# Kernel tuning notes

Measured on AMD Instinct MI355X. Metric: run time of the kernel, lower is better.

## Reference

```python
import jax, jax.numpy as jnp
import numpy as np

N, M, F, W = 600000, 300000, 128, 256  # points, masked points, grid feat_dim, net width


def _lin_init(k, fi, fo):
    k1, k2 = jax.random.split(k)
    s = 1.0 / np.sqrt(fi)
    return (jax.random.uniform(k1, (fi, fo), jnp.float32, -s, s),
            jax.random.uniform(k2, (fo,), jnp.float32, -s, s))


def setup_inputs() -> dict:
    key = jax.random.key(0)
    ks = jax.random.split(key, 24)
    # unique sorted indices emulate the boolean target_mask (static count M)
    idx = jnp.asarray(np.sort(np.random.RandomState(0).permutation(N)[:M]).astype(np.int32))
    inp = {
        "rays_pts_emb": jax.random.normal(ks[0], (N, 3), jnp.float32),
        "rotations_emb": jax.random.normal(ks[1], (N, 4), jnp.float32),
        "shs_emb": jax.random.normal(ks[2], (N, 16, 3), jnp.float32),
        "time_emb": jax.random.uniform(ks[3], (N, 1), jnp.float32),
        "h_emb": jax.random.uniform(ks[4], (N, 1), jnp.float32),
        "grid_sp": jax.random.normal(ks[5], (M, F), jnp.float32),
        "grid_st": jax.random.normal(ks[6], (M, F), jnp.float32),
        "idx": idx,
    }
    layers = [("sp", F, W), ("st", F, W), ("p1", W, W), ("p2", W, 9),
              ("r1", W, W), ("r2", W, 4), ("s1", W, W), ("s2", W, 48),
              ("w1", W, W), ("w2", W, 1), ("m1", W, W), ("m2", W, 1)]
    for i, (nm, fi, fo) in enumerate(layers):
        Wt, b = _lin_init(ks[7 + i], fi, fo)
        inp["W_" + nm] = Wt
        inp["b_" + nm] = b
    return inp


def _head(x, W1, b1, W2, b2):
    # nn.Sequential(ReLU, Linear, ReLU, Linear)
    h = jax.nn.relu(x)
    h = jax.nn.relu(h @ W1 + b1)
    return h @ W2 + b2


def reference(rays_pts_emb, rotations_emb, shs_emb, time_emb, h_emb, grid_sp, grid_st, idx,
              W_sp, b_sp, W_st, b_st, W_p1, b_p1, W_p2, b_p2, W_r1, b_r1, W_r2, b_r2,
              W_s1, b_s1, W_s2, b_s2, W_w1, b_w1, W_w2, b_w2, W_m1, b_m1, W_m2, b_m2):
    # encoders (Linear only, no activation)
    sp = grid_sp @ W_sp + b_sp            # [M, W]
    st = grid_st @ W_st + b_st            # [M, W]
    t = time_emb[0:1]                     # [1, 1]
    mint = 1.0 - t
    # position deformation: Bezier combination of 3 control offsets
    dx = _head(sp, W_p1, b_p1, W_p2, b_p2).reshape(-1, 3, 3)  # [M, 3, 3]
    delta = (3.0 * mint ** 2 * t * dx[:, 0]
             + 3.0 * mint * t ** 2 * dx[:, 1]
             + t ** 3 * dx[:, 2])                              # [M, 3]
    pts = rays_pts_emb.at[idx].add(delta)
    rotations = rotations_emb.at[idx].add(_head(st, W_r1, b_r1, W_r2, b_r2))
    shs = shs_emb.at[idx].add(_head(st, W_s1, b_s1, W_s2, b_s2).reshape(-1, 16, 3))
    # opacity gating
    w = _head(sp, W_w1, b_w1, W_w2, b_w2) ** 2                 # [M, 1]
    mu = jax.nn.sigmoid(_head(sp, W_m1, b_m1, W_m2, b_m2))     # [M, 1]
    opacity = h_emb.at[idx].set(h_emb[idx] * jnp.exp(-w * (t - mu) ** 2))
    return (pts, rotations, opacity, shs)
```

## Files before the change

### kernel.cpp

```cpp
#include <hip/hip_runtime.h>
#include <hip/hip_bf16.h>
#include <stdint.h>

#define M_ROWS 300000

typedef __attribute__((ext_vector_type(8)))  short bf16x8;
typedef __attribute__((ext_vector_type(16))) float f32x16;
typedef __attribute__((ext_vector_type(4)))  float f32x4;

union U4 { uint4 u; bf16x8 h; unsigned short us[8]; };

__device__ __forceinline__ unsigned short f2bf(float f) {
  union { float f; uint32_t u; } v; v.f = f;
  uint32_t r = v.u + 0x7fffu + ((v.u >> 16) & 1u);
  return (unsigned short)(r >> 16);
}
__device__ __forceinline__ uint32_t pk2(float lo, float hi) {
  return (uint32_t)f2bf(lo) | ((uint32_t)f2bf(hi) << 16);
}
__device__ __forceinline__ f32x4 ntload4(const float* p) {
  return __builtin_nontemporal_load((const f32x4*)p);
}
__device__ __forceinline__ void ntstore4(float* p, f32x4 v) {
  __builtin_nontemporal_store(v, (f32x4*)p);
}

#define T_SP 0
#define T_ST 64
#define T_P1 128
#define T_P2 256
#define T_R1 272
#define T_R2 400
#define T_S1 416
#define T_S2 544
#define T_W1 576
#define T_W2 704
#define T_M1 720
#define T_M2 848
#define T_TOT 864

__global__ void prep_w(const float* Wsp, const float* Wst, const float* Wp1, const float* Wp2,
                       const float* Wr1, const float* Wr2, const float* Ws1, const float* Ws2,
                       const float* Ww1, const float* Ww2, const float* Wm1, const float* Wm2,
                       uint4* ws) {
  int b = blockIdx.x, l = threadIdx.x;
  const int starts[12] = {T_SP,T_ST,T_P1,T_P2,T_R1,T_R2,T_S1,T_S2,T_W1,T_W2,T_M1,T_M2};
  const int Ks[12]     = {128,128,256,256,256,256,256,256,256,256,256,256};
  const int Cos[12]    = {256,256,256,9,256,4,256,48,256,1,256,1};
  const float* Wp[12]  = {Wsp,Wst,Wp1,Wp2,Wr1,Wr2,Ws1,Ws2,Ww1,Ww2,Wm1,Wm2};
  int m = 0;
  #pragma unroll
  for (int i = 1; i < 12; ++i) if (b >= starts[i]) m = i;
  int local = b - starts[m];
  int KT = Ks[m] >> 4;
  int n0 = local / KT, k0 = local - n0 * KT;
  int col = n0 * 32 + (l & 31);
  int kbase = k0 * 16 + (l >> 5) * 8;
  const float* W = Wp[m];
  int Co = Cos[m];
  U4 pk;
  #pragma unroll
  for (int j = 0; j < 8; ++j) {
    float v = (col < Co) ? W[(size_t)(kbase + j) * Co + col] : 0.0f;
    pk.us[j] = f2bf(v);
  }
  ws[(size_t)b * 64 + l] = pk.u;
}

__global__ void copy_emb(const float* pts, const float* rot, const float* h,
                         const float* shs, float* out) {
  long long stride = (long long)gridDim.x * blockDim.x;
  for (long long i = (long long)blockIdx.x * blockDim.x + threadIdx.x; i < 8400000LL; i += stride) {
    if (i < 450000) {
      ntstore4(out + i * 4, ntload4(pts + i * 4));
    } else if (i < 1050000) {
      f32x4 v = ntload4(rot + (i - 450000) * 4);
      *(f32x4*)(out + i * 4) = v;
    } else if (i < 1200000) {
      ntstore4(out + i * 4, ntload4(h + (i - 1050000) * 4));
    } else {
      f32x4 v = ntload4(shs + (i - 1200000) * 4);
      *(f32x4*)(out + i * 4) = v;
    }
  }
}

#define LSTR 512
__device__ __forceinline__ int lds_addr(int row, int cb) {
  return row * LSTR + (cb ^ ((row & 15) << 4));
}

__device__ __forceinline__ void loadX(const float* grid, int row0, int t, char* buf) {
  #pragma unroll
  for (int i = 0; i < 4; ++i) {
    int fi = i * 512 + t;
    int row = fi >> 5;
    int c4 = fi & 31;
    int gr = row0 + row; gr = gr < M_ROWS ? gr : (M_ROWS - 1);
    f32x4 v = ntload4(grid + (size_t)gr * 128 + c4 * 4);
    ushort4 p;
    p.x = f2bf(v.x); p.y = f2bf(v.y); p.z = f2bf(v.z); p.w = f2bf(v.w);
    *(ushort4*)(buf + lds_addr(row, c4 * 8)) = p;
  }
}

__device__ __forceinline__ void pre8(U4 (&d)[8], const uint4* base, int lane) {
  #pragma unroll
  for (int i = 0; i < 8; ++i) d[i].u = base[(size_t)i * 64 + lane];
}
__device__ __forceinline__ void pre4(U4 (&d)[8], const uint4* base, int lane) {
  #pragma unroll
  for (int i = 0; i < 4; ++i) d[i].u = base[(size_t)i * 64 + lane];
}
__device__ __forceinline__ void pre_s2(U4 (&d)[8], const uint4* wt, int kq, int lane) {
  #pragma unroll
  for (int kk = 0; kk < 4; ++kk)
    #pragma unroll
    for (int n = 0; n < 2; ++n)
      d[kk * 2 + n].u = wt[(size_t)((n * 16 + kq * 4 + kk) * 64) + lane];
}

__device__ __forceinline__ void mm_big8T(U4 (&b)[8], const char* inb, int k0, int arow, int khalf,
                                         f32x16& acc0, f32x16& acc1) {
  #pragma unroll
  for (int k = 0; k < 8; ++k) {
    bf16x8 x0 = *(const bf16x8*)(inb + lds_addr(arow, (k0 + k) * 32 + khalf));
    bf16x8 x1 = *(const bf16x8*)(inb + lds_addr(32 + arow, (k0 + k) * 32 + khalf));
    acc0 = __builtin_amdgcn_mfma_f32_32x32x16_bf16(b[k].h, x0, acc0, 0, 0, 0);
    acc1 = __builtin_amdgcn_mfma_f32_32x32x16_bf16(b[k].h, x1, acc1, 0, 0, 0);
  }
}

__device__ __forceinline__ void store_actT(char* outb, const float* bias, int wave, int lane,
                                           const f32x16& acc0, const f32x16& acc1) {
  const int xr = lane & 31;
  const int cb0 = wave * 32 + 4 * (lane >> 5);
  #pragma unroll
  for (int run = 0; run < 4; ++run) {
    const int c0 = cb0 + 8 * run;
    const float4 bv = *(const float4*)(bias + c0);
    uint2 w0, w1;
    w0.x = pk2(fmaxf(acc0[run * 4 + 0] + bv.x, 0.0f), fmaxf(acc0[run * 4 + 1] + bv.y, 0.0f));
    w0.y = pk2(fmaxf(acc0[run * 4 + 2] + bv.z, 0.0f), fmaxf(acc0[run * 4 + 3] + bv.w, 0.0f));
    w1.x = pk2(fmaxf(acc1[run * 4 + 0] + bv.x, 0.0f), fmaxf(acc1[run * 4 + 1] + bv.y, 0.0f));
    w1.y = pk2(fmaxf(acc1[run * 4 + 2] + bv.z, 0.0f), fmaxf(acc1[run * 4 + 3] + bv.w, 0.0f));
    *(uint2*)(outb + lds_addr(xr, c0 * 2)) = w0;
    *(uint2*)(outb + lds_addr(32 + xr, c0 * 2)) = w1;
  }
}

__device__ __forceinline__ void mm_head1(U4 (&b)[8], const char* inb, int rg, int kq, int khalf,
                                         int lane, f32x16& acc) {
  const int arow = rg * 32 + (lane & 31);
  #pragma unroll
  for (int kk = 0; kk < 4; ++kk) {
    bf16x8 a = *(const bf16x8*)(inb + lds_addr(arow, (kq * 4 + kk) * 32 + khalf));
    acc = __builtin_amdgcn_mfma_f32_32x32x16_bf16(a, b[kk].h, acc, 0, 0, 0);
  }
}

template<int COLS>
__device__ __forceinline__ void head_atomic(float* outsm, int rg, int lane, const f32x16& acc) {
  int col = lane & 31;
  if (col < COLS) {
    #pragma unroll
    for (int q = 0; q < 16; ++q) {
      int row = rg * 32 + (q & 3) + 8 * (q >> 2) + 4 * (lane >> 5);
      atomicAdd(&outsm[row * COLS + col], acc[q]);
    }
  }
}

__device__ __forceinline__ void rot_atomic_global(const f32x16& acc, int rg, int kq, int lane,
                                                  const int* sidx, int row0, const float* b_r2,
                                                  float* out) {
  int col = lane & 31;
  if (col < 4) {
    float bb = (kq == 0) ? b_r2[col] : 0.0f;
    #pragma unroll
    for (int q = 0; q < 16; ++q) {
      int row = rg * 32 + (q & 3) + 8 * (q >> 2) + 4 * (lane >> 5);
      if (row0 + row < M_ROWS) {
        atomicAdd(out + 1800000 + (size_t)sidx[row] * 4 + col, acc[q] + bb);
      }
    }
  }
}

__device__ __forceinline__ void shs_atomic_global(const f32x16& a0, const f32x16& a1,
                                                  int rg, int kq, int lane,
                                                  const int* sidx, int row0, const float* b_s2,
                                                  float* out) {
  int c = lane & 31;
  float bb0 = (kq == 0) ? b_s2[c] : 0.0f;
  float bb1 = (kq == 0 && c < 16) ? b_s2[32 + c] : 0.0f;
  #pragma unroll
  for (int q = 0; q < 16; ++q) {
    int row = rg * 32 + (q & 3) + 8 * (q >> 2) + 4 * (lane >> 5);
    if (row0 + row < M_ROWS) {
      size_t base = 4800000 + (size_t)sidx[row] * 48;
      atomicAdd(out + base + c, a0[q] + bb0);
      if (c < 16) atomicAdd(out + base + 32 + c, a1[q] + bb1);
    }
  }
}

__global__ void __launch_bounds__(512, 4) deform_main(
    const float* grid_sp, const float* grid_st, const int* idx,
    const float* rays, const float* rotq, const float* shs_in,
    const float* time_emb, const float* h_emb,
    const uint4* ws,
    const float* b_sp, const float* b_st, const float* b_p1, const float* b_p2,
    const float* b_r1, const float* b_r2, const float* b_s1, const float* b_s2,
    const float* b_w1, const float* b_w2, const float* b_m1, const float* b_m2,
    float* out) {
  __shared__ char bufA[32768];
  __shared__ char bufB[32768];
  __shared__ float smf[704];
  __shared__ int sidx[64];
  float* dxb = smf;
  float* wb  = smf + 576;
  float* mub = smf + 640;

  const int t = threadIdx.x;
  const int lane = t & 63;
  const int wave = t >> 6;
  const int rg = wave & 1;
  const int kq = wave >> 1;
  const int arow = lane & 31;
  const int khalf = (lane >> 5) * 16;
  const int row0 = blockIdx.x * 64;
  const float tt = time_emb[0];

  U4 b0[8], b1[8];
  pre8(b0, ws + (size_t)(T_SP + wave * 8) * 64, lane);

  if (t < 64) { int gr = row0 + t; sidx[t] = idx[gr < M_ROWS ? gr : (M_ROWS - 1)]; }
  if (t < 512) smf[t] = 0.0f;
  if (t < 192) smf[512 + t] = 0.0f;
  loadX(grid_sp, row0, t, bufA);
  __syncthreads();

  {
    f32x16 a0 = (f32x16)0.0f, a1 = (f32x16)0.0f;
    pre8(b1, ws + (size_t)(T_P1 + wave * 16) * 64, lane);
    __builtin_amdgcn_s_setprio(1);
    mm_big8T(b0, bufA, 0, arow, khalf, a0, a1);
    __builtin_amdgcn_s_setprio(0);
    store_actT(bufB, b_sp, wave, lane, a0, a1);
  }
  __syncthreads();

  {
    f32x16 a0 = (f32x16)0.0f, a1 = (f32x16)0.0f;
    pre8(b0, ws + (size_t)(T_P1 + wave * 16 + 8) * 64, lane);
    __builtin_amdgcn_s_setprio(1);
    mm_big8T(b1, bufB, 0, arow, khalf, a0, a1);
    __builtin_amdgcn_s_setprio(0);
    pre4(b1, ws + (size_t)(T_P2 + kq * 4) * 64, lane);
    __builtin_amdgcn_s_setprio(1);
    mm_big8T(b0, bufB, 8, arow, khalf, a0, a1);
    __builtin_amdgcn_s_setprio(0);
    store_actT(bufA, b_p1, wave, lane, a0, a1);
  }
  __syncthreads();

  {
    f32x16 hacc = (f32x16)0.0f;
    pre8(b0, ws + (size_t)(T_W1 + wave * 16) * 64, lane);
    __builtin_amdgcn_s_setprio(1);
    mm_head1(b1, bufA, rg, kq, khalf, lane, hacc);
    __builtin_amdgcn_s_setprio(0);
    head_atomic<9>(dxb, rg, lane, hacc);
  }
  __syncthreads();

  {
    f32x16 a0 = (f32x16)0.0f, a1 = (f32x16)0.0f;
    pre8(b1, ws + (size_t)(T_W1 + wave * 16 + 8) * 64, lane);
    __builtin_amdgcn_s_setprio(1);
    mm_big8T(b0, bufB, 0, arow, khalf, a0, a1);
    __builtin_amdgcn_s_setprio(0);
    pre4(b0, ws + (size_t)(T_W2 + kq * 4) * 64, lane);
    __builtin_amdgcn_s_setprio(1);
    mm_big8T(b1, bufB, 8, arow, khalf, a0, a1);
    __builtin_amdgcn_s_setprio(0);
    store_actT(bufA, b_w1, wave, lane, a0, a1);
  }
  __syncthreads();

  {
    f32x16 hacc = (f32x16)0.0f;
    pre8(b1, ws + (size_t)(T_M1 + wave * 16) * 64, lane);
    __builtin_amdgcn_s_setprio(1);
    mm_head1(b0, bufA, rg, kq, khalf, lane, hacc);
    __builtin_amdgcn_s_setprio(0);
    head_atomic<1>(wb, rg, lane, hacc);
  }
  __syncthreads();

  {
    f32x16 a0 = (f32x16)0.0f, a1 = (f32x16)0.0f;
    pre8(b0, ws + (size_t)(T_M1 + wave * 16 + 8) * 64, lane);
    __builtin_amdgcn_s_setprio(1);
    mm_big8T(b1, bufB, 0, arow, khalf, a0, a1);
    __builtin_amdgcn_s_setprio(0);
    pre4(b1, ws + (size_t)(T_M2 + kq * 4) * 64, lane);
    __builtin_amdgcn_s_setprio(1);
    mm_big8T(b0, bufB, 8, arow, khalf, a0, a1);
    __builtin_amdgcn_s_setprio(0);
    store_actT(bufA, b_m1, wave, lane, a0, a1);
  }
  __syncthreads();

  float pr = 0.0f, hv = 0.0f;
  {
    if (t < 256) {
      int row = t >> 2, sub = t & 3;
      int g = sidx[row];
      if (sub < 3) pr = rays[(size_t)g * 3 + sub]; else hv = h_emb[g];
    }
    loadX(grid_st, row0, t, bufB);
    f32x16 hacc = (f32x16)0.0f;
    __builtin_amdgcn_s_setprio(1);
    mm_head1(b1, bufA, rg, kq, khalf, lane, hacc);
    __builtin_amdgcn_s_setprio(0);
    pre8(b0, ws + (size_t)(T_ST + wave * 8) * 64, lane);
    head_atomic<1>(mub, rg, lane, hacc);
  }
  __syncthreads();

  {
    f32x16 a0 = (f32x16)0.0f, a1 = (f32x16)0.0f;
    pre8(b1, ws + (size_t)(T_R1 + wave * 16) * 64, lane);
    __builtin_amdgcn_s_setprio(1);
    mm_big8T(b0, bufB, 0, arow, khalf, a0, a1);
    __builtin_amdgcn_s_setprio(0);
    store_actT(bufA, b_st, wave, lane, a0, a1);
    if (t < 256) {
      int row = t >> 2, sub = t & 3;
      int gr = row0 + row;
      if (gr < M_ROWS) {
        int g = sidx[row];
        if (sub < 3) {
          float mt = 1.0f - tt;
          float c0 = 3.0f * mt * mt * tt, c1 = 3.0f * mt * tt * tt, c2 = tt * tt * tt;
          float d0 = dxb[row * 9 + sub]     + b_p2[sub];
          float d1 = dxb[row * 9 + 3 + sub] + b_p2[3 + sub];
          float d2 = dxb[row * 9 + 6 + sub] + b_p2[6 + sub];
          __builtin_nontemporal_store(pr + (c0 * d0 + c1 * d1 + c2 * d2),
                                      out + (size_t)g * 3 + sub);
        } else {
          float wr = wb[row] + b_w2[0];
          float mr = mub[row] + b_m2[0];
          float mu = 1.0f / (1.0f + expf(-mr));
          float dtm = tt - mu;
          __builtin_nontemporal_store(hv * expf(-(wr * wr) * dtm * dtm),
                                      out + 4200000 + (size_t)g);
        }
      }
    }
  }
  __syncthreads();

  {
    f32x16 a0 = (f32x16)0.0f, a1 = (f32x16)0.0f;
    pre8(b0, ws + (size_t)(T_R1 + wave * 16 + 8) * 64, lane);
    __builtin_amdgcn_s_setprio(1);
    mm_big8T(b1, bufA, 0, arow, khalf, a0, a1);
    __builtin_amdgcn_s_setprio(0);
    pre4(b1, ws + (size_t)(T_R2 + kq * 4) * 64, lane);
    __builtin_amdgcn_s_setprio(1);
    mm_big8T(b0, bufA, 8, arow, khalf, a0, a1);
    __builtin_amdgcn_s_setprio(0);
    store_actT(bufB, b_r1, wave, lane, a0, a1);
  }
  __syncthreads();

  {
    f32x16 hacc = (f32x16)0.0f;
    pre8(b0, ws + (size_t)(T_S1 + wave * 16) * 64, lane);
    __builtin_amdgcn_s_setprio(1);
    mm_head1(b1, bufB, rg, kq, khalf, lane, hacc);
    __builtin_amdgcn_s_setprio(0);
    rot_atomic_global(hacc, rg, kq, lane, sidx, row0, b_r2, out);
  }
  __syncthreads();

  {
    f32x16 a0 = (f32x16)0.0f, a1 = (f32x16)0.0f;
    pre8(b1, ws + (size_t)(T_S1 + wave * 16 + 8) * 64, lane);
    __builtin_amdgcn_s_setprio(1);
    mm_big8T(b0, bufA, 0, arow, khalf, a0, a1);
    __builtin_amdgcn_s_setprio(0);
    pre_s2(b0, ws + (size_t)T_S2 * 64, kq, lane);
    __builtin_amdgcn_s_setprio(1);
    mm_big8T(b1, bufA, 8, arow, khalf, a0, a1);
    __builtin_amdgcn_s_setprio(0);
    store_actT(bufB, b_s1, wave, lane, a0, a1);
  }
  __syncthreads();

  {
    f32x16 h0 = (f32x16)0.0f, h1 = (f32x16)0.0f;
    const int ar = rg * 32 + (lane & 31);
    __builtin_amdgcn_s_setprio(1);
    #pragma unroll
    for (int kk = 0; kk < 4; ++kk) {
      bf16x8 a = *(const bf16x8*)(bufB + lds_addr(ar, (kq * 4 + kk) * 32 + khalf));
      h0 = __builtin_amdgcn_mfma_f32_32x32x16_bf16(a, b0[kk * 2 + 0].h, h0, 0, 0, 0);
      h1 = __builtin_amdgcn_mfma_f32_32x32x16_bf16(a, b0[kk * 2 + 1].h, h1, 0, 0, 0);
    }
    __builtin_amdgcn_s_setprio(0);
    shs_atomic_global(h0, h1, rg, kq, lane, sidx, row0, b_s2, out);
  }
}

extern "C" void kernel_launch(void* const* d_in, const int* in_sizes, int n_in,
                              void* d_out, int out_size, void* d_ws, size_t ws_size,
                              hipStream_t stream) {
  const float* rays     = (const float*)d_in[0];
  const float* rotq     = (const float*)d_in[1];
  const float* shs      = (const float*)d_in[2];
  const float* time_emb = (const float*)d_in[3];
  const float* h_emb    = (const float*)d_in[4];
  const float* grid_sp  = (const float*)d_in[5];
  const float* grid_st  = (const float*)d_in[6];
  const int*   idx      = (const int*)d_in[7];
  uint4* ws = (uint4*)d_ws;

  prep_w<<<T_TOT, 64, 0, stream>>>(
      (const float*)d_in[8],  (const float*)d_in[10], (const float*)d_in[12], (const float*)d_in[14],
      (const float*)d_in[16], (const float*)d_in[18], (const float*)d_in[20], (const float*)d_in[22],
      (const float*)d_in[24], (const float*)d_in[26], (const float*)d_in[28], (const float*)d_in[30],
      ws);

  copy_emb<<<2048, 256, 0, stream>>>(rays, rotq, h_emb, shs, (float*)d_out);

  deform_main<<<(M_ROWS + 63) / 64, 512, 0, stream>>>(
      grid_sp, grid_st, idx, rays, rotq, shs, time_emb, h_emb, ws,
      (const float*)d_in[9],  (const float*)d_in[11], (const float*)d_in[13], (const float*)d_in[15],
      (const float*)d_in[17], (const float*)d_in[19], (const float*)d_in[21], (const float*)d_in[23],
      (const float*)d_in[25], (const float*)d_in[27], (const float*)d_in[29], (const float*)d_in[31],
      (float*)d_out);
}
```

Baseline: 708.1 us.

## Fuse passthrough embedding copies into main kernel using a mask bitmap

```diff
diff --git a/kernel.cpp b/kernel.cpp
--- a/kernel.cpp
+++ b/kernel.cpp
@@ -3,6 +3,7 @@
 #include <stdint.h>
 
 #define M_ROWS 300000
+#define NB_DEF 4688
 
 typedef __attribute__((ext_vector_type(8)))  short bf16x8;
 typedef __attribute__((ext_vector_type(16))) float f32x16;
@@ -23,6 +24,9 @@
 }
 __device__ __forceinline__ void ntstore4(float* p, f32x4 v) {
   __builtin_nontemporal_store(v, (f32x4*)p);
+}
+__device__ __forceinline__ bool bit_set(const uint32_t* bm, int r) {
+  return (bm[r >> 5] >> (r & 31)) & 1u;
 }
 
 #define T_SP 0
@@ -67,22 +71,10 @@
   ws[(size_t)b * 64 + l] = pk.u;
 }
 
-__global__ void copy_emb(const float* pts, const float* rot, const float* h,
-                         const float* shs, float* out) {
-  long long stride = (long long)gridDim.x * blockDim.x;
-  for (long long i = (long long)blockIdx.x * blockDim.x + threadIdx.x; i < 8400000LL; i += stride) {
-    if (i < 450000) {
-      ntstore4(out + i * 4, ntload4(pts + i * 4));
-    } else if (i < 1050000) {
-      f32x4 v = ntload4(rot + (i - 450000) * 4);
-      *(f32x4*)(out + i * 4) = v;
-    } else if (i < 1200000) {
-      ntstore4(out + i * 4, ntload4(h + (i - 1050000) * 4));
-    } else {
-      f32x4 v = ntload4(shs + (i - 1200000) * 4);
-      *(f32x4*)(out + i * 4) = v;
-    }
-  }
+__global__ void bm_zero(uint32_t* bm) { bm[blockIdx.x * 256 + threadIdx.x] = 0u; }
+__global__ void bm_set(const int* idx, uint32_t* bm) {
+  int i = blockIdx.x * 256 + threadIdx.x;
+  if (i < M_ROWS) { int g = idx[i]; atomicOr(&bm[g >> 5], 1u << (g & 31)); }
 }
 
 #define LSTR 512
@@ -209,7 +201,7 @@
     const float* grid_sp, const float* grid_st, const int* idx,
     const float* rays, const float* rotq, const float* shs_in,
     const float* time_emb, const float* h_emb,
-    const uint4* ws,
+    const uint4* ws, const uint32_t* bm,
     const float* b_sp, const float* b_st, const float* b_p1, const float* b_p2,
     const float* b_r1, const float* b_r2, const float* b_s1, const float* b_s2,
     const float* b_w1, const float* b_w2, const float* b_m1, const float* b_m2,
@@ -229,7 +221,8 @@
   const int kq = wave >> 1;
   const int arow = lane & 31;
   const int khalf = (lane >> 5) * 16;
-  const int row0 = blockIdx.x * 64;
+  const int bid = blockIdx.x;
+  const int row0 = bid * 64;
   const float tt = time_emb[0];
 
   U4 b0[8], b1[8];
@@ -244,6 +237,22 @@
   {
     f32x16 a0 = (f32x16)0.0f, a1 = (f32x16)0.0f;
     pre8(b1, ws + (size_t)(T_P1 + wave * 16) * 64, lane);
+    if (t < 64 && row0 + t < M_ROWS) {
+      int g = sidx[t];
+      *(float4*)(out + 1800000 + (size_t)g * 4) = *(const float4*)(rotq + (size_t)g * 4);
+    }
+    #pragma unroll
+    for (int i = 0; i < 2; ++i) {
+      int e = i * 512 + t;
+      if (e < 768) {
+        int r = e / 12, c = e - r * 12;
+        if (row0 + r < M_ROWS) {
+          int g = sidx[r];
+          *(float4*)(out + 4800000 + (size_t)g * 48 + c * 4) =
+              *(const float4*)(shs_in + (size_t)g * 48 + c * 4);
+        }
+      }
+    }
     __builtin_amdgcn_s_setprio(1);
     mm_big8T(b0, bufA, 0, arow, khalf, a0, a1);
     __builtin_amdgcn_s_setprio(0);
@@ -254,6 +263,20 @@
   {
     f32x16 a0 = (f32x16)0.0f, a1 = (f32x16)0.0f;
     pre8(b0, ws + (size_t)(T_P1 + wave * 16 + 8) * 64, lane);
+    {
+      long long c0 = (long long)bid * 1536;
+      #pragma unroll
+      for (int i = 0; i < 2; ++i) {
+        int j = i * 512 + t;
+        if (j < 768) {
+          long long c = c0 + j;
+          if (c < 7200000) {
+            int r = (int)(c / 12);
+            if (!bit_set(bm, r)) ntstore4(out + 4800000 + c * 4, ntload4(shs_in + c * 4));
+          }
+        }
+      }
+    }
     __builtin_amdgcn_s_setprio(1);
     mm_big8T(b1, bufB, 0, arow, khalf, a0, a1);
     __builtin_amdgcn_s_setprio(0);
@@ -278,6 +301,20 @@
   {
     f32x16 a0 = (f32x16)0.0f, a1 = (f32x16)0.0f;
     pre8(b1, ws + (size_t)(T_W1 + wave * 16 + 8) * 64, lane);
+    {
+      long long c0 = (long long)bid * 1536 + 768;
+      #pragma unroll
+      for (int i = 0; i < 2; ++i) {
+        int j = i * 512 + t;
+        if (j < 768) {
+          long long c = c0 + j;
+          if (c < 7200000) {
+            int r = (int)(c / 12);
+            if (!bit_set(bm, r)) ntstore4(out + 4800000 + c * 4, ntload4(shs_in + c * 4));
+          }
+        }
+      }
+    }
     __builtin_amdgcn_s_setprio(1);
     mm_big8T(b0, bufB, 0, arow, khalf, a0, a1);
     __builtin_amdgcn_s_setprio(0);
@@ -302,6 +339,21 @@
   {
     f32x16 a0 = (f32x16)0.0f, a1 = (f32x16)0.0f;
     pre8(b0, ws + (size_t)(T_M1 + wave * 16 + 8) * 64, lane);
+    if (t < 384) {
+      long long e = (long long)bid * 384 + t;
+      if (e < 1800000) {
+        int r = (int)(e / 3);
+        if (!bit_set(bm, r))
+          __builtin_nontemporal_store(__builtin_nontemporal_load(rays + e), out + e);
+      }
+    }
+    if (t < 128) {
+      long long c = (long long)bid * 128 + t;
+      if (c < 600000) {
+        int r = (int)c;
+        if (!bit_set(bm, r)) ntstore4(out + 1800000 + c * 4, ntload4(rotq + c * 4));
+      }
+    }
     __builtin_amdgcn_s_setprio(1);
     mm_big8T(b1, bufB, 0, arow, khalf, a0, a1);
     __builtin_amdgcn_s_setprio(0);
@@ -319,6 +371,15 @@
       int row = t >> 2, sub = t & 3;
       int g = sidx[row];
       if (sub < 3) pr = rays[(size_t)g * 3 + sub]; else hv = h_emb[g];
+    }
+    if (t >= 256 && t < 384) {
+      long long e = (long long)bid * 128 + (t - 256);
+      if (e < 600000) {
+        int r = (int)e;
+        if (!bit_set(bm, r))
+          __builtin_nontemporal_store(__builtin_nontemporal_load(h_emb + e),
+                                      out + 4200000 + e);
+      }
     }
     loadX(grid_st, row0, t, bufB);
     f32x16 hacc = (f32x16)0.0f;
@@ -428,6 +489,7 @@
   const float* grid_st  = (const float*)d_in[6];
   const int*   idx      = (const int*)d_in[7];
   uint4* ws = (uint4*)d_ws;
+  uint32_t* bm = (uint32_t*)((char*)d_ws + (size_t)T_TOT * 1024);
 
   prep_w<<<T_TOT, 64, 0, stream>>>(
       (const float*)d_in[8],  (const float*)d_in[10], (const float*)d_in[12], (const float*)d_in[14],
@@ -435,10 +497,11 @@
       (const float*)d_in[24], (const float*)d_in[26], (const float*)d_in[28], (const float*)d_in[30],
       ws);
 
-  copy_emb<<<2048, 256, 0, stream>>>(rays, rotq, h_emb, shs, (float*)d_out);
-
-  deform_main<<<(M_ROWS + 63) / 64, 512, 0, stream>>>(
-      grid_sp, grid_st, idx, rays, rotq, shs, time_emb, h_emb, ws,
+  bm_zero<<<75, 256, 0, stream>>>(bm);
+  bm_set<<<(M_ROWS + 255) / 256, 256, 0, stream>>>(idx, bm);
+
+  deform_main<<<NB_DEF, 512, 0, stream>>>(
+      grid_sp, grid_st, idx, rays, rotq, shs, time_emb, h_emb, ws, bm,
       (const float*)d_in[9],  (const float*)d_in[11], (const float*)d_in[13], (const float*)d_in[15],
       (const float*)d_in[17], (const float*)d_in[19], (const float*)d_in[21], (const float*)d_in[23],
       (const float*)d_in[25], (const float*)d_in[27], (const float*)d_in[29], (const float*)d_in[31],
```

New measurement: 944.4 us. 1.33x slower.

## Halve block row tile to 32 rows and repartition head work across waves

Applied to the files above, without the earlier changes.

```diff
diff --git a/kernel.cpp b/kernel.cpp
--- a/kernel.cpp
+++ b/kernel.cpp
@@ -92,12 +92,11 @@
 
 __device__ __forceinline__ void loadX(const float* grid, int row0, int t, char* buf) {
   #pragma unroll
-  for (int i = 0; i < 4; ++i) {
+  for (int i = 0; i < 2; ++i) {
     int fi = i * 512 + t;
     int row = fi >> 5;
     int c4 = fi & 31;
-    int gr = row0 + row; gr = gr < M_ROWS ? gr : (M_ROWS - 1);
-    f32x4 v = ntload4(grid + (size_t)gr * 128 + c4 * 4);
+    f32x4 v = ntload4(grid + (size_t)(row0 + row) * 128 + c4 * 4);
     ushort4 p;
     p.x = f2bf(v.x); p.y = f2bf(v.y); p.z = f2bf(v.z); p.w = f2bf(v.w);
     *(ushort4*)(buf + lds_addr(row, c4 * 8)) = p;
@@ -112,95 +111,85 @@
   #pragma unroll
   for (int i = 0; i < 4; ++i) d[i].u = base[(size_t)i * 64 + lane];
 }
-__device__ __forceinline__ void pre_s2(U4 (&d)[8], const uint4* wt, int kq, int lane) {
+__device__ __forceinline__ void pre2(U4 (&d)[8], const uint4* base, int lane) {
+  d[0].u = base[lane]; d[1].u = base[64 + lane];
+}
+__device__ __forceinline__ void pre_s2(U4 (&d)[8], const uint4* wt, int ct2, int kqs, int lane) {
   #pragma unroll
   for (int kk = 0; kk < 4; ++kk)
-    #pragma unroll
-    for (int n = 0; n < 2; ++n)
-      d[kk * 2 + n].u = wt[(size_t)((n * 16 + kq * 4 + kk) * 64) + lane];
-}
-
-__device__ __forceinline__ void mm_big8T(U4 (&b)[8], const char* inb, int k0, int arow, int khalf,
-                                         f32x16& acc0, f32x16& acc1) {
+    d[kk].u = wt[(size_t)((ct2 * 16 + kqs * 4 + kk) * 64) + lane];
+}
+
+__device__ __forceinline__ void mm_big8S(U4 (&b)[8], const char* inb, int k0, int arow, int khalf,
+                                         f32x16& acc) {
   #pragma unroll
   for (int k = 0; k < 8; ++k) {
-    bf16x8 x0 = *(const bf16x8*)(inb + lds_addr(arow, (k0 + k) * 32 + khalf));
-    bf16x8 x1 = *(const bf16x8*)(inb + lds_addr(32 + arow, (k0 + k) * 32 + khalf));
-    acc0 = __builtin_amdgcn_mfma_f32_32x32x16_bf16(b[k].h, x0, acc0, 0, 0, 0);
-    acc1 = __builtin_amdgcn_mfma_f32_32x32x16_bf16(b[k].h, x1, acc1, 0, 0, 0);
-  }
-}
-
-__device__ __forceinline__ void store_actT(char* outb, const float* bias, int wave, int lane,
-                                           const f32x16& acc0, const f32x16& acc1) {
+    bf16x8 x = *(const bf16x8*)(inb + lds_addr(arow, (k0 + k) * 32 + khalf));
+    acc = __builtin_amdgcn_mfma_f32_32x32x16_bf16(b[k].h, x, acc, 0, 0, 0);
+  }
+}
+
+__device__ __forceinline__ void store_actS(char* outb, const float* bias, int wave, int lane,
+                                           const f32x16& acc) {
   const int xr = lane & 31;
   const int cb0 = wave * 32 + 4 * (lane >> 5);
   #pragma unroll
   for (int run = 0; run < 4; ++run) {
     const int c0 = cb0 + 8 * run;
     const float4 bv = *(const float4*)(bias + c0);
-    uint2 w0, w1;
-    w0.x = pk2(fmaxf(acc0[run * 4 + 0] + bv.x, 0.0f), fmaxf(acc0[run * 4 + 1] + bv.y, 0.0f));
-    w0.y = pk2(fmaxf(acc0[run * 4 + 2] + bv.z, 0.0f), fmaxf(acc0[run * 4 + 3] + bv.w, 0.0f));
-    w1.x = pk2(fmaxf(acc1[run * 4 + 0] + bv.x, 0.0f), fmaxf(acc1[run * 4 + 1] + bv.y, 0.0f));
-    w1.y = pk2(fmaxf(acc1[run * 4 + 2] + bv.z, 0.0f), fmaxf(acc1[run * 4 + 3] + bv.w, 0.0f));
-    *(uint2*)(outb + lds_addr(xr, c0 * 2)) = w0;
-    *(uint2*)(outb + lds_addr(32 + xr, c0 * 2)) = w1;
-  }
-}
-
-__device__ __forceinline__ void mm_head1(U4 (&b)[8], const char* inb, int rg, int kq, int khalf,
-                                         int lane, f32x16& acc) {
-  const int arow = rg * 32 + (lane & 31);
-  #pragma unroll
-  for (int kk = 0; kk < 4; ++kk) {
-    bf16x8 a = *(const bf16x8*)(inb + lds_addr(arow, (kq * 4 + kk) * 32 + khalf));
-    acc = __builtin_amdgcn_mfma_f32_32x32x16_bf16(a, b[kk].h, acc, 0, 0, 0);
-  }
+    uint2 w;
+    w.x = pk2(fmaxf(acc[run * 4 + 0] + bv.x, 0.0f), fmaxf(acc[run * 4 + 1] + bv.y, 0.0f));
+    w.y = pk2(fmaxf(acc[run * 4 + 2] + bv.z, 0.0f), fmaxf(acc[run * 4 + 3] + bv.w, 0.0f));
+    *(uint2*)(outb + lds_addr(xr, c0 * 2)) = w;
+  }
+}
+
+__device__ __forceinline__ void mm_head2t(U4 (&b)[8], const char* inb, int kq8, int khalf,
+                                          int lane, f32x16& acc) {
+  const int arow = lane & 31;
+  bf16x8 a0 = *(const bf16x8*)(inb + lds_addr(arow, (kq8 * 2 + 0) * 32 + khalf));
+  bf16x8 a1 = *(const bf16x8*)(inb + lds_addr(arow, (kq8 * 2 + 1) * 32 + khalf));
+  acc = __builtin_amdgcn_mfma_f32_32x32x16_bf16(a0, b[0].h, acc, 0, 0, 0);
+  acc = __builtin_amdgcn_mfma_f32_32x32x16_bf16(a1, b[1].h, acc, 0, 0, 0);
 }
 
 template<int COLS>
-__device__ __forceinline__ void head_atomic(float* outsm, int rg, int lane, const f32x16& acc) {
+__device__ __forceinline__ void head_atomic(float* outsm, int lane, const f32x16& acc) {
   int col = lane & 31;
   if (col < COLS) {
     #pragma unroll
     for (int q = 0; q < 16; ++q) {
-      int row = rg * 32 + (q & 3) + 8 * (q >> 2) + 4 * (lane >> 5);
+      int row = (q & 3) + 8 * (q >> 2) + 4 * (lane >> 5);
       atomicAdd(&outsm[row * COLS + col], acc[q]);
     }
   }
 }
 
-__device__ __forceinline__ void rot_atomic_global(const f32x16& acc, int rg, int kq, int lane,
-                                                  const int* sidx, int row0, const float* b_r2,
+__device__ __forceinline__ void rot_atomic_global(const f32x16& acc, int kq4, int lane,
+                                                  const int* sidx, const float* b_r2,
                                                   float* out) {
   int col = lane & 31;
   if (col < 4) {
-    float bb = (kq == 0) ? b_r2[col] : 0.0f;
+    float bb = (kq4 == 0) ? b_r2[col] : 0.0f;
     #pragma unroll
     for (int q = 0; q < 16; ++q) {
-      int row = rg * 32 + (q & 3) + 8 * (q >> 2) + 4 * (lane >> 5);
-      if (row0 + row < M_ROWS) {
-        atomicAdd(out + 1800000 + (size_t)sidx[row] * 4 + col, acc[q] + bb);
-      }
-    }
-  }
-}
-
-__device__ __forceinline__ void shs_atomic_global(const f32x16& a0, const f32x16& a1,
-                                                  int rg, int kq, int lane,
-                                                  const int* sidx, int row0, const float* b_s2,
+      int row = (q & 3) + 8 * (q >> 2) + 4 * (lane >> 5);
+      atomicAdd(out + 1800000 + (size_t)sidx[row] * 4 + col, acc[q] + bb);
+    }
+  }
+}
+
+__device__ __forceinline__ void shs_atomic_global(const f32x16& acc, int ct2, int kqs, int lane,
+                                                  const int* sidx, const float* b_s2,
                                                   float* out) {
   int c = lane & 31;
-  float bb0 = (kq == 0) ? b_s2[c] : 0.0f;
-  float bb1 = (kq == 0 && c < 16) ? b_s2[32 + c] : 0.0f;
-  #pragma unroll
-  for (int q = 0; q < 16; ++q) {
-    int row = rg * 32 + (q & 3) + 8 * (q >> 2) + 4 * (lane >> 5);
-    if (row0 + row < M_ROWS) {
-      size_t base = 4800000 + (size_t)sidx[row] * 48;
-      atomicAdd(out + base + c, a0[q] + bb0);
-      if (c < 16) atomicAdd(out + base + 32 + c, a1[q] + bb1);
+  int col = ct2 * 32 + c;
+  if (col < 48) {
+    float bb = (kqs == 0) ? b_s2[col] : 0.0f;
+    #pragma unroll
+    for (int q = 0; q < 16; ++q) {
+      int row = (q & 3) + 8 * (q >> 2) + 4 * (lane >> 5);
+      atomicAdd(out + 4800000 + (size_t)sidx[row] * 48 + col, acc[q] + bb);
     }
   }
 }
@@ -214,54 +203,55 @@
     const float* b_r1, const float* b_r2, const float* b_s1, const float* b_s2,
     const float* b_w1, const float* b_w2, const float* b_m1, const float* b_m2,
     float* out) {
-  __shared__ char bufA[32768];
-  __shared__ char bufB[32768];
-  __shared__ float smf[704];
-  __shared__ int sidx[64];
+  __shared__ char bufA[16384];
+  __shared__ char bufB[16384];
+  __shared__ float smf[352];
+  __shared__ int sidx[32];
   float* dxb = smf;
-  float* wb  = smf + 576;
-  float* mub = smf + 640;
+  float* wb  = smf + 288;
+  float* mub = smf + 320;
 
   const int t = threadIdx.x;
   const int lane = t & 63;
   const int wave = t >> 6;
-  const int rg = wave & 1;
-  const int kq = wave >> 1;
+  const int kq8 = wave;
+  const int kq4 = wave & 3;
+  const int ct2 = wave & 1;
+  const int kqs = wave >> 1;
   const int arow = lane & 31;
   const int khalf = (lane >> 5) * 16;
-  const int row0 = blockIdx.x * 64;
+  const int row0 = blockIdx.x * 32;
   const float tt = time_emb[0];
 
   U4 b0[8], b1[8];
   pre8(b0, ws + (size_t)(T_SP + wave * 8) * 64, lane);
 
-  if (t < 64) { int gr = row0 + t; sidx[t] = idx[gr < M_ROWS ? gr : (M_ROWS - 1)]; }
-  if (t < 512) smf[t] = 0.0f;
-  if (t < 192) smf[512 + t] = 0.0f;
+  if (t < 32) sidx[t] = idx[row0 + t];
+  if (t < 352) smf[t] = 0.0f;
   loadX(grid_sp, row0, t, bufA);
   __syncthreads();
 
   {
-    f32x16 a0 = (f32x16)0.0f, a1 = (f32x16)0.0f;
+    f32x16 acc = (f32x16)0.0f;
     pre8(b1, ws + (size_t)(T_P1 + wave * 16) * 64, lane);
     __builtin_amdgcn_s_setprio(1);
-    mm_big8T(b0, bufA, 0, arow, khalf, a0, a1);
-    __builtin_amdgcn_s_setprio(0);
-    store_actT(bufB, b_sp, wave, lane, a0, a1);
-  }
-  __syncthreads();
-
-  {
-    f32x16 a0 = (f32x16)0.0f, a1 = (f32x16)0.0f;
+    mm_big8S(b0, bufA, 0, arow, khalf, acc);
+    __builtin_amdgcn_s_setprio(0);
+    store_actS(bufB, b_sp, wave, lane, acc);
+  }
+  __syncthreads();
+
+  {
+    f32x16 acc = (f32x16)0.0f;
     pre8(b0, ws + (size_t)(T_P1 + wave * 16 + 8) * 64, lane);
     __builtin_amdgcn_s_setprio(1);
-    mm_big8T(b1, bufB, 0, arow, khalf, a0, a1);
-    __builtin_amdgcn_s_setprio(0);
-    pre4(b1, ws + (size_t)(T_P2 + kq * 4) * 64, lane);
-    __builtin_amdgcn_s_setprio(1);
-    mm_big8T(b0, bufB, 8, arow, khalf, a0, a1);
-    __builtin_amdgcn_s_setprio(0);
-    store_actT(bufA, b_p1, wave, lane, a0, a1);
+    mm_big8S(b1, bufB, 0, arow, khalf, acc);
+    __builtin_amdgcn_s_setprio(0);
+    pre2(b1, ws + (size_t)(T_P2 + kq8 * 2) * 64, lane);
+    __builtin_amdgcn_s_setprio(1);
+    mm_big8S(b0, bufB, 8, arow, khalf, acc);
+    __builtin_amdgcn_s_setprio(0);
+    store_actS(bufA, b_p1, wave, lane, acc);
   }
   __syncthreads();
 
@@ -269,23 +259,23 @@
     f32x16 hacc = (f32x16)0.0f;
     pre8(b0, ws + (size_t)(T_W1 + wave * 16) * 64, lane);
     __builtin_amdgcn_s_setprio(1);
-    mm_head1(b1, bufA, rg, kq, khalf, lane, hacc);
-    __builtin_amdgcn_s_setprio(0);
-    head_atomic<9>(dxb, rg, lane, hacc);
-  }
-  __syncthreads();
-
-  {
-    f32x16 a0 = (f32x16)0.0f, a1 = (f32x16)0.0f;
+    mm_head2t(b1, bufA, kq8, khalf, lane, hacc);
+    __builtin_amdgcn_s_setprio(0);
+    head_atomic<9>(dxb, lane, hacc);
+  }
+  __syncthreads();
+
+  {
+    f32x16 acc = (f32x16)0.0f;
     pre8(b1, ws + (size_t)(T_W1 + wave * 16 + 8) * 64, lane);
     __builtin_amdgcn_s_setprio(1);
-    mm_big8T(b0, bufB, 0, arow, khalf, a0, a1);
-    __builtin_amdgcn_s_setprio(0);
-    pre4(b0, ws + (size_t)(T_W2 + kq * 4) * 64, lane);
-    __builtin_amdgcn_s_setprio(1);
-    mm_big8T(b1, bufB, 8, arow, khalf, a0, a1);
-    __builtin_amdgcn_s_setprio(0);
-    store_actT(bufA, b_w1, wave, lane, a0, a1);
+    mm_big8S(b0, bufB, 0, arow, khalf, acc);
+    __builtin_amdgcn_s_setprio(0);
+    pre2(b0, ws + (size_t)(T_W2 + kq8 * 2) * 64, lane);
+    __builtin_amdgcn_s_setprio(1);
+    mm_big8S(b1, bufB, 8, arow, khalf, acc);
+    __builtin_amdgcn_s_setprio(0);
+    store_actS(bufA, b_w1, wave, lane, acc);
   }
   __syncthreads();
 
@@ -293,29 +283,29 @@
     f32x16 hacc = (f32x16)0.0f;
     pre8(b1, ws + (size_t)(T_M1 + wave * 16) * 64, lane);
     __builtin_amdgcn_s_setprio(1);
-    mm_head1(b0, bufA, rg, kq, khalf, lane, hacc);
-    __builtin_amdgcn_s_setprio(0);
-    head_atomic<1>(wb, rg, lane, hacc);
-  }
-  __syncthreads();
-
-  {
-    f32x16 a0 = (f32x16)0.0f, a1 = (f32x16)0.0f;
+    mm_head2t(b0, bufA, kq8, khalf, lane, hacc);
+    __builtin_amdgcn_s_setprio(0);
+    head_atomic<1>(wb, lane, hacc);
+  }
+  __syncthreads();
+
+  {
+    f32x16 acc = (f32x16)0.0f;
     pre8(b0, ws + (size_t)(T_M1 + wave * 16 + 8) * 64, lane);
     __builtin_amdgcn_s_setprio(1);
-    mm_big8T(b1, bufB, 0, arow, khalf, a0, a1);
-    __builtin_amdgcn_s_setprio(0);
-    pre4(b1, ws + (size_t)(T_M2 + kq * 4) * 64, lane);
-    __builtin_amdgcn_s_setprio(1);
-    mm_big8T(b0, bufB, 8, arow, khalf, a0, a1);
-    __builtin_amdgcn_s_setprio(0);
-    store_actT(bufA, b_m1, wave, lane, a0, a1);
+    mm_big8S(b1, bufB, 0, arow, khalf, acc);
+    __builtin_amdgcn_s_setprio(0);
+    pre2(b1, ws + (size_t)(T_M2 + kq8 * 2) * 64, lane);
+    __builtin_amdgcn_s_setprio(1);
+    mm_big8S(b0, bufB, 8, arow, khalf, acc);
+    __builtin_amdgcn_s_setprio(0);
+    store_actS(bufA, b_m1, wave, lane, acc);
   }
   __syncthreads();
 
   float pr = 0.0f, hv = 0.0f;
   {
-    if (t < 256) {
+    if (t < 128) {
       int row = t >> 2, sub = t & 3;
       int g = sidx[row];
       if (sub < 3) pr = rays[(size_t)g * 3 + sub]; else hv = h_emb[g];
@@ -323,96 +313,99 @@
     loadX(grid_st, row0, t, bufB);
     f32x16 hacc = (f32x16)0.0f;
     __builtin_amdgcn_s_setprio(1);
-    mm_head1(b1, bufA, rg, kq, khalf, lane, hacc);
+    mm_head2t(b1, bufA, kq8, khalf, lane, hacc);
     __builtin_amdgcn_s_setprio(0);
     pre8(b0, ws + (size_t)(T_ST + wave * 8) * 64, lane);
-    head_atomic<1>(mub, rg, lane, hacc);
-  }
-  __syncthreads();
-
-  {
-    f32x16 a0 = (f32x16)0.0f, a1 = (f32x16)0.0f;
+    head_atomic<1>(mub, lane, hacc);
+  }
+  __syncthreads();
+
+  {
+    f32x16 acc = (f32x16)0.0f;
     pre8(b1, ws + (size_t)(T_R1 + wave * 16) * 64, lane);
     __builtin_amdgcn_s_setprio(1);
-    mm_big8T(b0, bufB, 0, arow, khalf, a0, a1);
-    __builtin_amdgcn_s_setprio(0);
-    store_actT(bufA, b_st, wave, lane, a0, a1);
-    if (t < 256) {
+    mm_big8S(b0, bufB, 0, arow, khalf, acc);
+    __builtin_amdgcn_s_setprio(0);
+    store_actS(bufA, b_st, wave, lane, acc);
+    if (t < 128) {
       int row = t >> 2, sub = t & 3;
-      int gr = row0 + row;
-      if (gr < M_ROWS) {
-        int g = sidx[row];
-        if (sub < 3) {
-          float mt = 1.0f - tt;
-          float c0 = 3.0f * mt * mt * tt, c1 = 3.0f * mt * tt * tt, c2 = tt * tt * tt;
-          float d0 = dxb[row * 9 + sub]     + b_p2[sub];
-          float d1 = dxb[row * 9 + 3 + sub] + b_p2[3 + sub];
-          float d2 = dxb[row * 9 + 6 + sub] + b_p2[6 + sub];
-          __builtin_nontemporal_store(pr + (c0 * d0 + c1 * d1 + c2 * d2),
-                                      out + (size_t)g * 3 + sub);
-        } else {
-          float wr = wb[row] + b_w2[0];
-          float mr = mub[row] + b_m2[0];
-          float mu = 1.0f / (1.0f + expf(-mr));
-          float dtm = tt - mu;
-          __builtin_nontemporal_store(hv * expf(-(wr * wr) * dtm * dtm),
-                                      out + 4200000 + (size_t)g);
-        }
+      int g = sidx[row];
+      if (sub < 3) {
+        float mt = 1.0f - tt;
+        float c0 = 3.0f * mt * mt * tt, c1 = 3.0f * mt * tt * tt, c2 = tt * tt * tt;
+        float d0 = dxb[row * 9 + sub]     + b_p2[sub];
+        float d1 = dxb[row * 9 + 3 + sub] + b_p2[3 + sub];
+        float d2 = dxb[row * 9 + 6 + sub] + b_p2[6 + sub];
+        __builtin_nontemporal_store(pr + (c0 * d0 + c1 * d1 + c2 * d2),
+                                    out + (size_t)g * 3 + sub);
+      } else {
+        float wr = wb[row] + b_w2[0];
+        float mr = mub[row] + b_m2[0];
+        float mu = 1.0f / (1.0f + expf(-mr));
+        float dtm = tt - mu;
+        __builtin_nontemporal_store(hv * expf(-(wr * wr) * dtm * dtm),
+                                    out + 4200000 + (size_t)g);
       }
     }
   }
   __syncthreads();
 
   {
-    f32x16 a0 = (f32x16)0.0f, a1 = (f32x16)0.0f;
+    f32x16 acc = (f32x16)0.0f;
     pre8(b0, ws + (size_t)(T_R1 + wave * 16 + 8) * 64, lane);
     __builtin_amdgcn_s_setprio(1);
-    mm_big8T(b1, bufA, 0, arow, khalf, a0, a1);
-    __builtin_amdgcn_s_setprio(0);
-    pre4(b1, ws + (size_t)(T_R2 + kq * 4) * 64, lane);
-    __builtin_amdgcn_s_setprio(1);
-    mm_big8T(b0, bufA, 8, arow, khalf, a0, a1);
-    __builtin_amdgcn_s_setprio(0);
-    store_actT(bufB, b_r1, wave, lane, a0, a1);
+    mm_big8S(b1, bufA, 0, arow, khalf, acc);
+    __builtin_amdgcn_s_setprio(0);
+    pre4(b1, ws + (size_t)(T_R2 + kq4 * 4) * 64, lane);
+    __builtin_amdgcn_s_setprio(1);
+    mm_big8S(b0, bufA, 8, arow, khalf, acc);
+    __builtin_amdgcn_s_setprio(0);
+    store_actS(bufB, b_r1, wave, lane, acc);
+  }
+  __syncthreads();
+
+  {
+    if (wave < 4) {
+      f32x16 hacc = (f32x16)0.0f;
+      const int ar = lane & 31;
+      __builtin_amdgcn_s_setprio(1);
+      #pragma unroll
+      for (int kk = 0; kk < 4; ++kk) {
+        bf16x8 a = *(const bf16x8*)(bufB + lds_addr(ar, (kq4 * 4 + kk) * 32 + khalf));
+        hacc = __builtin_amdgcn_mfma_f32_32x32x16_bf16(a, b1[kk].h, hacc, 0, 0, 0);
+      }
+      __builtin_amdgcn_s_setprio(0);
+      rot_atomic_global(hacc, kq4, lane, sidx, b_r2, out);
+    }
+    pre8(b0, ws + (size_t)(T_S1 + wave * 16) * 64, lane);
+  }
+  __syncthreads();
+
+  {
+    f32x16 acc = (f32x16)0.0f;
+    pre8(b1, ws + (size_t)(T_S1 + wave * 16 + 8) * 64, lane);
+    __builtin_amdgcn_s_setprio(1);
+    mm_big8S(b0, bufA, 0, arow, khalf, acc);
+    __builtin_amdgcn_s_setprio(0);
+    pre_s2(b0, ws + (size_t)T_S2 * 64, ct2, kqs, lane);
+    __builtin_amdgcn_s_setprio(1);
+    mm_big8S(b1, bufA, 8, arow, khalf, acc);
+    __builtin_amdgcn_s_setprio(0);
+    store_actS(bufB, b_s1, wave, lane, acc);
   }
   __syncthreads();
 
   {
     f32x16 hacc = (f32x16)0.0f;
-    pre8(b0, ws + (size_t)(T_S1 + wave * 16) * 64, lane);
-    __builtin_amdgcn_s_setprio(1);
-    mm_head1(b1, bufB, rg, kq, khalf, lane, hacc);
-    __builtin_amdgcn_s_setprio(0);
-    rot_atomic_global(hacc, rg, kq, lane, sidx, row0, b_r2, out);
-  }
-  __syncthreads();
-
-  {
-    f32x16 a0 = (f32x16)0.0f, a1 = (f32x16)0.0f;
-    pre8(b1, ws + (size_t)(T_S1 + wave * 16 + 8) * 64, lane);
-    __builtin_amdgcn_s_setprio(1);
-    mm_big8T(b0, bufA, 0, arow, khalf, a0, a1);
-    __builtin_amdgcn_s_setprio(0);
-    pre_s2(b0, ws + (size_t)T_S2 * 64, kq, lane);
-    __builtin_amdgcn_s_setprio(1);
-    mm_big8T(b1, bufA, 8, arow, khalf, a0, a1);
-    __builtin_amdgcn_s_setprio(0);
-    store_actT(bufB, b_s1, wave, lane, a0, a1);
-  }
-  __syncthreads();
-
-  {
-    f32x16 h0 = (f32x16)0.0f, h1 = (f32x16)0.0f;
-    const int ar = rg * 32 + (lane & 31);
+    const int ar = lane & 31;
     __builtin_amdgcn_s_setprio(1);
     #pragma unroll
     for (int kk = 0; kk < 4; ++kk) {
-      bf16x8 a = *(const bf16x8*)(bufB + lds_addr(ar, (kq * 4 + kk) * 32 + khalf));
-      h0 = __builtin_amdgcn_mfma_f32_32x32x16_bf16(a, b0[kk * 2 + 0].h, h0, 0, 0, 0);
-      h1 = __builtin_amdgcn_mfma_f32_32x32x16_bf16(a, b0[kk * 2 + 1].h, h1, 0, 0, 0);
-    }
-    __builtin_amdgcn_s_setprio(0);
-    shs_atomic_global(h0, h1, rg, kq, lane, sidx, row0, b_s2, out);
+      bf16x8 a = *(const bf16x8*)(bufB + lds_addr(ar, (kqs * 4 + kk) * 32 + khalf));
+      hacc = __builtin_amdgcn_mfma_f32_32x32x16_bf16(a, b0[kk].h, hacc, 0, 0, 0);
+    }
+    __builtin_amdgcn_s_setprio(0);
+    shs_atomic_global(hacc, ct2, kqs, lane, sidx, b_s2, out);
   }
 }
 
@@ -437,7 +430,7 @@
 
   copy_emb<<<2048, 256, 0, stream>>>(rays, rotq, h_emb, shs, (float*)d_out);
 
-  deform_main<<<(M_ROWS + 63) / 64, 512, 0, stream>>>(
+  deform_main<<<M_ROWS / 32, 512, 0, stream>>>(
       grid_sp, grid_st, idx, rays, rotq, shs, time_emb, h_emb, ws,
       (const float*)d_in[9],  (const float*)d_in[11], (const float*)d_in[13], (const float*)d_in[15],
       (const float*)d_in[17], (const float*)d_in[19], (const float*)d_in[21], (const float*)d_in[23],
```

New measurement: 664.3 us, median of 2. 6.2% less time.
